# Kernel optimization log

Measured on AMD Instinct MI355X. Metric: run time of the kernel, lower is better.

The kernel has to match this reference:

```python
import jax, jax.numpy as jnp
import numpy as np

N_SRC = 32768
N_DST = 32768
E = 524288
SRC_D = 64
DST_D = 64
EDGE_D = 16
OUT_D = 128
HEADS = 8
IN_D = SRC_D + DST_D + EDGE_D  # 144


def _lin_init(k, i, o):
    return jax.random.normal(k, (i, o), jnp.float32) * (1.0 / np.sqrt(i))


def setup_inputs() -> dict:
    key = jax.random.key(0)
    ks = jax.random.split(key, 12)
    return {
        "x_src": jax.random.normal(ks[0], (N_SRC, SRC_D), jnp.float32),
        "x_dst": jax.random.normal(ks[1], (N_DST, DST_D), jnp.float32),
        "edge_attr": jax.random.normal(ks[2], (E, EDGE_D), jnp.float32),
        "edge_index": jax.random.randint(ks[3], (2, E), 0, N_DST, dtype=jnp.int64),
        "q": jax.random.uniform(ks[4], (1, OUT_D), jnp.float32) * 0.1,
        "k_w0": _lin_init(ks[5], IN_D, OUT_D), "k_b0": jnp.zeros((OUT_D,), jnp.float32),
        "k_w1": _lin_init(ks[6], OUT_D, OUT_D), "k_b1": jnp.zeros((OUT_D,), jnp.float32),
        "v_w0": _lin_init(ks[7], IN_D, OUT_D), "v_b0": jnp.zeros((OUT_D,), jnp.float32),
        "v_w1": _lin_init(ks[8], OUT_D, OUT_D), "v_b1": jnp.zeros((OUT_D,), jnp.float32),
        "o_w0": _lin_init(ks[9], OUT_D, OUT_D), "o_b0": jnp.zeros((OUT_D,), jnp.float32),
        "o_w1": _lin_init(ks[10], OUT_D, OUT_D), "o_b1": jnp.zeros((OUT_D,), jnp.float32),
    }


def _res_stack(x, w0, b0, w1, b1, last_activation):
    # ResidualStack(n_residuals=2): input linear + relu, then one residual linear block
    h = jax.nn.relu(x @ w0 + b0)
    h = h + (h @ w1 + b1)
    return jax.nn.relu(h) if last_activation else h


def reference(x_src, x_dst, edge_attr, edge_index, q,
              k_w0, k_b0, k_w1, k_b1,
              v_w0, v_b0, v_w1, v_b1,
              o_w0, o_b0, o_w1, o_b1):
    src, dst = edge_index[0], edge_index[1]
    # gather per-edge features: [E, IN_D]
    x = jnp.concatenate([x_src[src], x_dst[dst], edge_attr], axis=-1)
    k = _res_stack(x, k_w0, k_b0, k_w1, k_b1, False)   # [E, OUT_D]
    v = _res_stack(x, v_w0, v_b0, v_w1, v_b1, False)   # [E, OUT_D]
    d = OUT_D // HEADS
    qh = q.reshape(HEADS, d)
    kh = k.reshape(E, HEADS, d)
    scores = jnp.einsum('hd,ehd->eh', qh, kh) / jnp.sqrt(jnp.float32(d))  # [E, H]
    # segment softmax over destination-node neighborhoods
    seg_max = jax.ops.segment_max(scores, dst, num_segments=N_DST)
    seg_max = jnp.where(jnp.isfinite(seg_max), seg_max, jnp.float32(0.0))
    ex = jnp.exp(scores - seg_max[dst])
    denom = jax.ops.segment_sum(ex, dst, num_segments=N_DST)
    attn = ex / (denom[dst] + jnp.float32(1e-16))      # [E, H]
    msg = (attn[:, :, None] * v.reshape(E, HEADS, d)).reshape(E, OUT_D)
    aggr = jax.ops.segment_sum(msg, dst, num_segments=N_DST)  # [N_DST, OUT_D]
    out = _res_stack(jax.nn.relu(aggr), o_w0, o_b0, o_w1, o_b1, True)
    return out
```

## Files before the change

### kernel.cpp

```cpp
#include <hip/hip_runtime.h>
#include <math.h>

#define NSRC 32768
#define NDST 32768
#define NE 524288
#define SRC_D 64
#define DST_D 64
#define EDGE_D 16
#define IN_DIM 144
#define OUT_DIM 128
#define HEADS 8
#define HD 16

__global__ __launch_bounds__(128) void build_A_kernel(
    const float* __restrict__ q, const float* __restrict__ k_w1,
    const float* __restrict__ k_b1, float* __restrict__ A, float* __restrict__ C)
{
    const int j = threadIdx.x;
    #pragma unroll
    for (int h = 0; h < HEADS; ++h) {
        float s = 0.f;
        #pragma unroll
        for (int d = 0; d < HD; ++d)
            s = fmaf(k_w1[j*OUT_DIM + h*HD + d], q[h*HD + d], s);
        if ((j >> 4) == h) s += q[j];
        A[j*HEADS + h] = 0.25f * s;
    }
    if (j < HEADS) {
        float s = 0.f;
        #pragma unroll
        for (int d = 0; d < HD; ++d) s = fmaf(q[j*HD + d], k_b1[j*HD + d], s);
        C[j] = 0.25f * s;
    }
}

__global__ __launch_bounds__(256) void edge_kernel(
    const float* __restrict__ x_src, const float* __restrict__ x_dst,
    const float* __restrict__ e_attr, const int* __restrict__ eidx,
    const float* __restrict__ k_w0, const float* __restrict__ k_b0,
    const float* __restrict__ v_w0, const float* __restrict__ v_b0,
    const float* __restrict__ v_w1, const float* __restrict__ v_b1,
    const float* __restrict__ A, const float* __restrict__ C,
    float* __restrict__ acc_g, float* __restrict__ denom_g)
{
    __shared__ float xs[32][IN_DIM];
    __shared__ float Hs[32][2*OUT_DIM];
    __shared__ float exs[32][HEADS];
    __shared__ int   dsts[32];

    const int t = threadIdx.x;
    const int e0 = blockIdx.x * 32;

    {
        const int g = t >> 3, l8 = t & 7;
        const int e = e0 + g;
        const int si = eidx[e];
        const int di = eidx[NE + e];
        if (l8 == 0) dsts[g] = di;
        const float4* ps = (const float4*)(x_src + (size_t)si * SRC_D);
        float4 a0 = ps[l8*2+0], a1 = ps[l8*2+1];
        *(float4*)&xs[g][l8*8+0] = a0;
        *(float4*)&xs[g][l8*8+4] = a1;
        const float4* pd = (const float4*)(x_dst + (size_t)di * DST_D);
        float4 b0 = pd[l8*2+0], b1 = pd[l8*2+1];
        *(float4*)&xs[g][SRC_D + l8*8+0] = b0;
        *(float4*)&xs[g][SRC_D + l8*8+4] = b1;
        const float2* pe = (const float2*)(e_attr + (size_t)e * EDGE_D);
        float2 c0 = pe[l8];
        *(float2*)&xs[g][SRC_D + DST_D + l8*2] = c0;
    }
    __syncthreads();

    {
        const float* __restrict__ W0 = (t < OUT_DIM) ? k_w0 : v_w0;
        const float* __restrict__ B0 = (t < OUT_DIM) ? k_b0 : v_b0;
        const int c = t & (OUT_DIM-1);
        float acc[32];
        #pragma unroll
        for (int e = 0; e < 32; ++e) acc[e] = 0.f;
        for (int i = 0; i < IN_DIM; i += 4) {
            const float w0v = W0[(i+0)*OUT_DIM + c];
            const float w1v = W0[(i+1)*OUT_DIM + c];
            const float w2v = W0[(i+2)*OUT_DIM + c];
            const float w3v = W0[(i+3)*OUT_DIM + c];
            #pragma unroll
            for (int e = 0; e < 32; ++e) {
                const float4 xv = *(const float4*)&xs[e][i];
                acc[e] = fmaf(xv.x, w0v, acc[e]);
                acc[e] = fmaf(xv.y, w1v, acc[e]);
                acc[e] = fmaf(xv.z, w2v, acc[e]);
                acc[e] = fmaf(xv.w, w3v, acc[e]);
            }
        }
        const float bv = B0[c];
        #pragma unroll
        for (int e = 0; e < 32; ++e) {
            Hs[e][t] = fmaxf(acc[e] + bv, 0.f);
        }
    }
    __syncthreads();

    const int cc = t & (OUT_DIM-1);
    const int half = t >> 7;

    float vacc[16];
    #pragma unroll
    for (int e2 = 0; e2 < 16; ++e2) vacc[e2] = 0.f;
    for (int j = 0; j < OUT_DIM; j += 4) {
        const float w0v = v_w1[(j+0)*OUT_DIM + cc];
        const float w1v = v_w1[(j+1)*OUT_DIM + cc];
        const float w2v = v_w1[(j+2)*OUT_DIM + cc];
        const float w3v = v_w1[(j+3)*OUT_DIM + cc];
        #pragma unroll
        for (int e2 = 0; e2 < 16; ++e2) {
            const float4 hv = *(const float4*)&Hs[half*16 + e2][OUT_DIM + j];
            vacc[e2] = fmaf(hv.x, w0v, vacc[e2]);
            vacc[e2] = fmaf(hv.y, w1v, vacc[e2]);
            vacc[e2] = fmaf(hv.z, w2v, vacc[e2]);
            vacc[e2] = fmaf(hv.w, w3v, vacc[e2]);
        }
    }

    {
        const int se = t >> 3;
        const int sh = t & 7;
        float s = C[sh];
        for (int j = 0; j < OUT_DIM; j += 4) {
            const float4 hk = *(const float4*)&Hs[se][j];
            s = fmaf(hk.x, A[(j+0)*HEADS + sh], s);
            s = fmaf(hk.y, A[(j+1)*HEADS + sh], s);
            s = fmaf(hk.z, A[(j+2)*HEADS + sh], s);
            s = fmaf(hk.w, A[(j+3)*HEADS + sh], s);
        }
        const float ex = __expf(s);
        exs[se][sh] = ex;
        atomicAdd(&denom_g[(size_t)dsts[se]*HEADS + sh], ex);
    }
    __syncthreads();

    {
        const float bv = v_b1[cc];
        #pragma unroll
        for (int e2 = 0; e2 < 16; ++e2) {
            const int e = half*16 + e2;
            const float v = Hs[e][OUT_DIM + cc] + vacc[e2] + bv;
            const float m = exs[e][cc >> 4] * v;
            atomicAdd(&acc_g[(size_t)dsts[e]*OUT_DIM + cc], m);
        }
    }
}

__global__ __launch_bounds__(256) void node_kernel(
    const float* __restrict__ acc_g, const float* __restrict__ denom_g,
    const float* __restrict__ o_w0, const float* __restrict__ o_b0,
    const float* __restrict__ o_w1, const float* __restrict__ o_b1,
    float* __restrict__ out)
{
    __shared__ float as[32][OUT_DIM];
    __shared__ float hs[32][OUT_DIM];
    const int t = threadIdx.x;
    const int n0 = blockIdx.x * 32;

    for (int r = t; r < 32*32; r += 256) {
        const int n = r >> 5, c4 = r & 31;
        float4 a = *(const float4*)&acc_g[(size_t)(n0+n)*OUT_DIM + c4*4];
        const float d = denom_g[(size_t)(n0+n)*HEADS + (c4 >> 2)] + 1e-16f;
        a.x = fmaxf(a.x / d, 0.f);
        a.y = fmaxf(a.y / d, 0.f);
        a.z = fmaxf(a.z / d, 0.f);
        a.w = fmaxf(a.w / d, 0.f);
        *(float4*)&as[n][c4*4] = a;
    }
    __syncthreads();

    const int cc = t & (OUT_DIM-1);
    const int half = t >> 7;
    float hreg[16];
    {
        float acc1[16];
        #pragma unroll
        for (int e2 = 0; e2 < 16; ++e2) acc1[e2] = 0.f;
        for (int j = 0; j < OUT_DIM; j += 4) {
            const float w0v = o_w0[(j+0)*OUT_DIM + cc];
            const float w1v = o_w0[(j+1)*OUT_DIM + cc];
            const float w2v = o_w0[(j+2)*OUT_DIM + cc];
            const float w3v = o_w0[(j+3)*OUT_DIM + cc];
            #pragma unroll
            for (int e2 = 0; e2 < 16; ++e2) {
                const float4 av = *(const float4*)&as[half*16 + e2][j];
                acc1[e2] = fmaf(av.x, w0v, acc1[e2]);
                acc1[e2] = fmaf(av.y, w1v, acc1[e2]);
                acc1[e2] = fmaf(av.z, w2v, acc1[e2]);
                acc1[e2] = fmaf(av.w, w3v, acc1[e2]);
            }
        }
        const float bv = o_b0[cc];
        #pragma unroll
        for (int e2 = 0; e2 < 16; ++e2) {
            float h = fmaxf(acc1[e2] + bv, 0.f);
            hreg[e2] = h;
            hs[half*16 + e2][cc] = h;
        }
    }
    __syncthreads();
    {
        float acc2[16];
        #pragma unroll
        for (int e2 = 0; e2 < 16; ++e2) acc2[e2] = 0.f;
        for (int j = 0; j < OUT_DIM; j += 4) {
            const float w0v = o_w1[(j+0)*OUT_DIM + cc];
            const float w1v = o_w1[(j+1)*OUT_DIM + cc];
            const float w2v = o_w1[(j+2)*OUT_DIM + cc];
            const float w3v = o_w1[(j+3)*OUT_DIM + cc];
            #pragma unroll
            for (int e2 = 0; e2 < 16; ++e2) {
                const float4 hv = *(const float4*)&hs[half*16 + e2][j];
                acc2[e2] = fmaf(hv.x, w0v, acc2[e2]);
                acc2[e2] = fmaf(hv.y, w1v, acc2[e2]);
                acc2[e2] = fmaf(hv.z, w2v, acc2[e2]);
                acc2[e2] = fmaf(hv.w, w3v, acc2[e2]);
            }
        }
        const float bv = o_b1[cc];
        #pragma unroll
        for (int e2 = 0; e2 < 16; ++e2) {
            const int n = n0 + half*16 + e2;
            out[(size_t)n*OUT_DIM + cc] = fmaxf(hreg[e2] + acc2[e2] + bv, 0.f);
        }
    }
}

extern "C" void kernel_launch(void* const* d_in, const int* in_sizes, int n_in,
                              void* d_out, int out_size, void* d_ws, size_t ws_size,
                              hipStream_t stream) {
    const float* x_src  = (const float*)d_in[0];
    const float* x_dst  = (const float*)d_in[1];
    const float* e_attr = (const float*)d_in[2];
    const int*   eidx   = (const int*)  d_in[3];
    const float* q      = (const float*)d_in[4];
    const float* k_w0   = (const float*)d_in[5];
    const float* k_b0   = (const float*)d_in[6];
    const float* k_w1   = (const float*)d_in[7];
    const float* k_b1   = (const float*)d_in[8];
    const float* v_w0   = (const float*)d_in[9];
    const float* v_b0   = (const float*)d_in[10];
    const float* v_w1   = (const float*)d_in[11];
    const float* v_b1   = (const float*)d_in[12];
    const float* o_w0   = (const float*)d_in[13];
    const float* o_b0   = (const float*)d_in[14];
    const float* o_w1   = (const float*)d_in[15];
    const float* o_b1   = (const float*)d_in[16];
    float* out = (float*)d_out;

    float* acc_g   = (float*)d_ws;
    float* denom_g = acc_g + (size_t)NDST*OUT_DIM;
    float* A       = denom_g + (size_t)NDST*HEADS;
    float* C       = A + 128*HEADS;

    hipMemsetAsync(d_ws, 0, ((size_t)NDST*OUT_DIM + (size_t)NDST*HEADS)*sizeof(float), stream);

    build_A_kernel<<<1, 128, 0, stream>>>(q, k_w1, k_b1, A, C);
    edge_kernel<<<NE/32, 256, 0, stream>>>(x_src, x_dst, e_attr, eidx,
                                           k_w0, k_b0, v_w0, v_b0, v_w1, v_b1,
                                           A, C, acc_g, denom_g);
    node_kernel<<<NDST/32, 256, 0, stream>>>(acc_g, denom_g,
                                             o_w0, o_b0, o_w1, o_b1, out);
}
```

Baseline: 1.356 ms.

## Retile edge MLP to 4-column register blocks with float4 weight loads

The per-edge first-layer and value second-layer matmuls are re-tiled so each thread computes a 4-column by 8-edge (or 4-edge) register block, using float4 weight loads instead of scalar ones. This cuts the number of shared-memory reads of the activations and global weight loads per FMA. The score projection matrix is also stored transposed so each head's coefficients load as float4, and the Hs row is padded to change LDS bank mapping. The atomic scatter now issues four atomics per thread per edge on contiguous columns instead of one, so the total atomic count is unchanged.

```diff
diff --git a/kernel.cpp b/kernel.cpp
--- a/kernel.cpp
+++ b/kernel.cpp
@@ -12,9 +12,12 @@
 #define HEADS 8
 #define HD 16
 
+#define HS_LD 264
+
 __global__ __launch_bounds__(128) void build_A_kernel(
     const float* __restrict__ q, const float* __restrict__ k_w1,
-    const float* __restrict__ k_b1, float* __restrict__ A, float* __restrict__ C)
+    const float* __restrict__ k_b1, float* __restrict__ A, float* __restrict__ C,
+    float* __restrict__ At)
 {
     const int j = threadIdx.x;
     #pragma unroll
@@ -24,7 +27,9 @@
         for (int d = 0; d < HD; ++d)
             s = fmaf(k_w1[j*OUT_DIM + h*HD + d], q[h*HD + d], s);
         if ((j >> 4) == h) s += q[j];
-        A[j*HEADS + h] = 0.25f * s;
+        const float a = 0.25f * s;
+        A[j*HEADS + h] = a;
+        At[h*OUT_DIM + j] = a;
     }
     if (j < HEADS) {
         float s = 0.f;
@@ -40,11 +45,11 @@
     const float* __restrict__ k_w0, const float* __restrict__ k_b0,
     const float* __restrict__ v_w0, const float* __restrict__ v_b0,
     const float* __restrict__ v_w1, const float* __restrict__ v_b1,
-    const float* __restrict__ A, const float* __restrict__ C,
+    const float* __restrict__ At, const float* __restrict__ C,
     float* __restrict__ acc_g, float* __restrict__ denom_g)
 {
     __shared__ float xs[32][IN_DIM];
-    __shared__ float Hs[32][2*OUT_DIM];
+    __shared__ float Hs[32][HS_LD];
     __shared__ float exs[32][HEADS];
     __shared__ int   dsts[32];
 
@@ -66,71 +71,113 @@
         *(float4*)&xs[g][SRC_D + l8*8+0] = b0;
         *(float4*)&xs[g][SRC_D + l8*8+4] = b1;
         const float2* pe = (const float2*)(e_attr + (size_t)e * EDGE_D);
-        float2 c0 = pe[l8];
-        *(float2*)&xs[g][SRC_D + DST_D + l8*2] = c0;
-    }
-    __syncthreads();
-
-    {
-        const float* __restrict__ W0 = (t < OUT_DIM) ? k_w0 : v_w0;
-        const float* __restrict__ B0 = (t < OUT_DIM) ? k_b0 : v_b0;
-        const int c = t & (OUT_DIM-1);
-        float acc[32];
-        #pragma unroll
-        for (int e = 0; e < 32; ++e) acc[e] = 0.f;
+        float2 c0v = pe[l8];
+        *(float2*)&xs[g][SRC_D + DST_D + l8*2] = c0v;
+    }
+    __syncthreads();
+
+    {
+        const int cq = t & 63;
+        const int c0 = cq * 4;
+        const int g  = t >> 6;
+        const bool isK = (c0 < OUT_DIM);
+        const float4* __restrict__ Wf4 =
+            (const float4*)(isK ? k_w0 : v_w0) + ((isK ? c0 : c0 - OUT_DIM) >> 2);
+        const float4 bias = *((const float4*)(isK ? k_b0 : v_b0) + ((isK ? c0 : c0 - OUT_DIM) >> 2));
+
+        float4 acc[8];
+        #pragma unroll
+        for (int e = 0; e < 8; ++e) acc[e] = make_float4(0.f, 0.f, 0.f, 0.f);
+
+        #pragma unroll 4
         for (int i = 0; i < IN_DIM; i += 4) {
-            const float w0v = W0[(i+0)*OUT_DIM + c];
-            const float w1v = W0[(i+1)*OUT_DIM + c];
-            const float w2v = W0[(i+2)*OUT_DIM + c];
-            const float w3v = W0[(i+3)*OUT_DIM + c];
+            const float4 wa = Wf4[(i+0) * (OUT_DIM/4)];
+            const float4 wb = Wf4[(i+1) * (OUT_DIM/4)];
+            const float4 wc = Wf4[(i+2) * (OUT_DIM/4)];
+            const float4 wd = Wf4[(i+3) * (OUT_DIM/4)];
             #pragma unroll
-            for (int e = 0; e < 32; ++e) {
-                const float4 xv = *(const float4*)&xs[e][i];
-                acc[e] = fmaf(xv.x, w0v, acc[e]);
-                acc[e] = fmaf(xv.y, w1v, acc[e]);
-                acc[e] = fmaf(xv.z, w2v, acc[e]);
-                acc[e] = fmaf(xv.w, w3v, acc[e]);
+            for (int e = 0; e < 8; ++e) {
+                const float4 xv = *(const float4*)&xs[g*8 + e][i];
+                acc[e].x = fmaf(xv.x, wa.x, acc[e].x);
+                acc[e].y = fmaf(xv.x, wa.y, acc[e].y);
+                acc[e].z = fmaf(xv.x, wa.z, acc[e].z);
+                acc[e].w = fmaf(xv.x, wa.w, acc[e].w);
+                acc[e].x = fmaf(xv.y, wb.x, acc[e].x);
+                acc[e].y = fmaf(xv.y, wb.y, acc[e].y);
+                acc[e].z = fmaf(xv.y, wb.z, acc[e].z);
+                acc[e].w = fmaf(xv.y, wb.w, acc[e].w);
+                acc[e].x = fmaf(xv.z, wc.x, acc[e].x);
+                acc[e].y = fmaf(xv.z, wc.y, acc[e].y);
+                acc[e].z = fmaf(xv.z, wc.z, acc[e].z);
+                acc[e].w = fmaf(xv.z, wc.w, acc[e].w);
+                acc[e].x = fmaf(xv.w, wd.x, acc[e].x);
+                acc[e].y = fmaf(xv.w, wd.y, acc[e].y);
+                acc[e].z = fmaf(xv.w, wd.z, acc[e].z);
+                acc[e].w = fmaf(xv.w, wd.w, acc[e].w);
             }
         }
-        const float bv = B0[c];
-        #pragma unroll
-        for (int e = 0; e < 32; ++e) {
-            Hs[e][t] = fmaxf(acc[e] + bv, 0.f);
-        }
-    }
-    __syncthreads();
-
-    const int cc = t & (OUT_DIM-1);
-    const int half = t >> 7;
-
-    float vacc[16];
-    #pragma unroll
-    for (int e2 = 0; e2 < 16; ++e2) vacc[e2] = 0.f;
-    for (int j = 0; j < OUT_DIM; j += 4) {
-        const float w0v = v_w1[(j+0)*OUT_DIM + cc];
-        const float w1v = v_w1[(j+1)*OUT_DIM + cc];
-        const float w2v = v_w1[(j+2)*OUT_DIM + cc];
-        const float w3v = v_w1[(j+3)*OUT_DIM + cc];
-        #pragma unroll
-        for (int e2 = 0; e2 < 16; ++e2) {
-            const float4 hv = *(const float4*)&Hs[half*16 + e2][OUT_DIM + j];
-            vacc[e2] = fmaf(hv.x, w0v, vacc[e2]);
-            vacc[e2] = fmaf(hv.y, w1v, vacc[e2]);
-            vacc[e2] = fmaf(hv.z, w2v, vacc[e2]);
-            vacc[e2] = fmaf(hv.w, w3v, vacc[e2]);
+        #pragma unroll
+        for (int e = 0; e < 8; ++e) {
+            float4 h;
+            h.x = fmaxf(acc[e].x + bias.x, 0.f);
+            h.y = fmaxf(acc[e].y + bias.y, 0.f);
+            h.z = fmaxf(acc[e].z + bias.z, 0.f);
+            h.w = fmaxf(acc[e].w + bias.w, 0.f);
+            *(float4*)&Hs[g*8 + e][c0] = h;
+        }
+    }
+    __syncthreads();
+
+    const int cq2 = t & 31;
+    const int c0v = cq2 * 4;
+    const int g2  = t >> 5;
+    float4 vacc[4];
+    {
+        const float4* __restrict__ Vf4 = (const float4*)v_w1 + cq2;
+        #pragma unroll
+        for (int e = 0; e < 4; ++e) vacc[e] = make_float4(0.f, 0.f, 0.f, 0.f);
+        #pragma unroll 4
+        for (int j = 0; j < OUT_DIM; j += 4) {
+            const float4 wa = Vf4[(j+0) * (OUT_DIM/4)];
+            const float4 wb = Vf4[(j+1) * (OUT_DIM/4)];
+            const float4 wc = Vf4[(j+2) * (OUT_DIM/4)];
+            const float4 wd = Vf4[(j+3) * (OUT_DIM/4)];
+            #pragma unroll
+            for (int e = 0; e < 4; ++e) {
+                const float4 hv = *(const float4*)&Hs[g2*4 + e][OUT_DIM + j];
+                vacc[e].x = fmaf(hv.x, wa.x, vacc[e].x);
+                vacc[e].y = fmaf(hv.x, wa.y, vacc[e].y);
+                vacc[e].z = fmaf(hv.x, wa.z, vacc[e].z);
+                vacc[e].w = fmaf(hv.x, wa.w, vacc[e].w);
+                vacc[e].x = fmaf(hv.y, wb.x, vacc[e].x);
+                vacc[e].y = fmaf(hv.y, wb.y, vacc[e].y);
+                vacc[e].z = fmaf(hv.y, wb.z, vacc[e].z);
+                vacc[e].w = fmaf(hv.y, wb.w, vacc[e].w);
+                vacc[e].x = fmaf(hv.z, wc.x, vacc[e].x);
+                vacc[e].y = fmaf(hv.z, wc.y, vacc[e].y);
+                vacc[e].z = fmaf(hv.z, wc.z, vacc[e].z);
+                vacc[e].w = fmaf(hv.z, wc.w, vacc[e].w);
+                vacc[e].x = fmaf(hv.w, wd.x, vacc[e].x);
+                vacc[e].y = fmaf(hv.w, wd.y, vacc[e].y);
+                vacc[e].z = fmaf(hv.w, wd.z, vacc[e].z);
+                vacc[e].w = fmaf(hv.w, wd.w, vacc[e].w);
+            }
         }
     }
 
     {
         const int se = t >> 3;
         const int sh = t & 7;
+        const float4* __restrict__ At4 = (const float4*)(At + sh * OUT_DIM);
         float s = C[sh];
+        #pragma unroll 4
         for (int j = 0; j < OUT_DIM; j += 4) {
             const float4 hk = *(const float4*)&Hs[se][j];
-            s = fmaf(hk.x, A[(j+0)*HEADS + sh], s);
-            s = fmaf(hk.y, A[(j+1)*HEADS + sh], s);
-            s = fmaf(hk.z, A[(j+2)*HEADS + sh], s);
-            s = fmaf(hk.w, A[(j+3)*HEADS + sh], s);
+            const float4 av = At4[j >> 2];
+            s = fmaf(hk.x, av.x, s);
+            s = fmaf(hk.y, av.y, s);
+            s = fmaf(hk.z, av.z, s);
+            s = fmaf(hk.w, av.w, s);
         }
         const float ex = __expf(s);
         exs[se][sh] = ex;
@@ -139,13 +186,18 @@
     __syncthreads();
 
     {
-        const float bv = v_b1[cc];
-        #pragma unroll
-        for (int e2 = 0; e2 < 16; ++e2) {
-            const int e = half*16 + e2;
-            const float v = Hs[e][OUT_DIM + cc] + vacc[e2] + bv;
-            const float m = exs[e][cc >> 4] * v;
-            atomicAdd(&acc_g[(size_t)dsts[e]*OUT_DIM + cc], m);
+        const float4 bv = *((const float4*)v_b1 + cq2);
+        const int h = c0v >> 4;
+        #pragma unroll
+        for (int e = 0; e < 4; ++e) {
+            const int ee = g2*4 + e;
+            const float4 hv = *(const float4*)&Hs[ee][OUT_DIM + c0v];
+            const float ex = exs[ee][h];
+            const size_t base = (size_t)dsts[ee]*OUT_DIM + c0v;
+            atomicAdd(&acc_g[base+0], ex * (hv.x + vacc[e].x + bv.x));
+            atomicAdd(&acc_g[base+1], ex * (hv.y + vacc[e].y + bv.y));
+            atomicAdd(&acc_g[base+2], ex * (hv.z + vacc[e].z + bv.z));
+            atomicAdd(&acc_g[base+3], ex * (hv.w + vacc[e].w + bv.w));
         }
     }
 }
@@ -256,13 +308,14 @@
     float* denom_g = acc_g + (size_t)NDST*OUT_DIM;
     float* A       = denom_g + (size_t)NDST*HEADS;
     float* C       = A + 128*HEADS;
+    float* At      = C + 8;
 
     hipMemsetAsync(d_ws, 0, ((size_t)NDST*OUT_DIM + (size_t)NDST*HEADS)*sizeof(float), stream);
 
-    build_A_kernel<<<1, 128, 0, stream>>>(q, k_w1, k_b1, A, C);
+    build_A_kernel<<<1, 128, 0, stream>>>(q, k_w1, k_b1, A, C, At);
     edge_kernel<<<NE/32, 256, 0, stream>>>(x_src, x_dst, e_attr, eidx,
                                            k_w0, k_b0, v_w0, v_b0, v_w1, v_b1,
-                                           A, C, acc_g, denom_g);
+                                           At, C, acc_g, denom_g);
     node_kernel<<<NDST/32, 256, 0, stream>>>(acc_g, denom_g,
                                              o_w0, o_b0, o_w1, o_b1, out);
 }
```

Measured after the change: 1.224 ms. 1.11x faster.
